# Performance work log

Hardware: AMD Instinct MI355X
Metric: run time of the kernel (lower is better)

## Reference

```python
import jax, jax.numpy as jnp
import numpy as np

WIN = 1022       # window_length == frame_length == fft_length
HOP = 256        # hop_length
SIG_LEN = 33216  # signal_length
FACTOR = 2       # downsampling factor
T_IN = 127       # input STFT frames
B = 64
L_OLA = (T_IN - 1) * HOP + WIN  # 33278, length produced by inverse_stft

# indices kept after the strided deletion (evens < SIG_LEN, plus OLA tail beyond SIG_LEN)
KEEP = np.concatenate([np.arange(0, SIG_LEN, FACTOR), np.arange(SIG_LEN, L_OLA)])
L_OUT = KEEP.shape[0]                # 16670
T_OUT = 1 + (L_OUT - WIN) // HOP     # 62 output STFT frames

def _hann(n):
    # periodic Hann, matches tf.signal.hann_window default
    return (0.5 - 0.5 * np.cos(2.0 * np.pi * np.arange(n) / n)).astype(np.float32)

def _synth_window():
    # tf.signal.inverse_stft_window_fn(HOP): w / overlap-added w^2 (periodic form)
    w = _hann(WIN)
    d = w * w
    overlaps = -(-WIN // HOP)
    d = np.pad(d, (0, overlaps * HOP - WIN))
    d = d.reshape(-1, HOP).sum(0)      # per-phase sum of squares
    d = np.tile(d, overlaps)[:WIN]
    return (w / d).astype(np.float32)

WINDOW = jnp.asarray(_hann(WIN))
SYNTH = jnp.asarray(_synth_window())
OLA_IDX = jnp.asarray((np.arange(T_IN)[:, None] * HOP + np.arange(WIN)[None, :]).reshape(-1))
FRAME_IDX = jnp.asarray(np.arange(T_OUT)[:, None] * HOP + np.arange(WIN)[None, :])
KEEP_J = jnp.asarray(KEEP)

def setup_inputs() -> dict:
    key = jax.random.key(0)
    return {"inputs": jax.random.normal(key, (B, 512, T_IN, 2), dtype=jnp.float32)}

def reference(inputs):
    # inputs: [B, 512, T, 2] (real/imag stacked STFT)
    stfts = jax.lax.complex(inputs[..., 0], inputs[..., 1])   # [B, 512, T]
    stfts = jnp.transpose(stfts, (0, 2, 1))                   # [B, T, 512]
    # inverse_stft: irfft per frame, apply synthesis window, overlap-add
    frames = jnp.fft.irfft(stfts, n=WIN, axis=-1) * SYNTH
    b = frames.shape[0]
    sig = jnp.zeros((b, L_OLA), frames.dtype).at[:, OLA_IDX].add(frames.reshape(b, -1))
    # strided index deletion (the unstack/del/stack loop) == single gather
    sig = sig[:, KEEP_J]                                      # [B, 16670]
    # forward STFT
    fr = sig[:, FRAME_IDX] * WINDOW
    S = jnp.fft.rfft(fr, n=WIN, axis=-1)                      # [B, T_OUT, 512]
    S = jnp.transpose(S, (0, 2, 1))                           # [B, 512, T_OUT]
    return jnp.stack([jnp.real(S), jnp.imag(S)], axis=-1)     # [B, 512, T_OUT, 2]
```

## Files before the change

### kernel.cpp

```cpp
#include <hip/hip_runtime.h>


#define WIN       1022
#define HOP       256
#define T_IN      127
#define NB        64
#define NPAD      1024
#define NE        512
#define T_OUT     62
#define HALF_KEPT 16608
#define L_USE     16638
#define ROWS1     8128
#define ROWS1P    8192
#define ROWS2     3968
#define ROWS2P    4096
#define TWO_PI_F  6.28318530717958647692f

typedef _Float16 half8 __attribute__((ext_vector_type(8)));
typedef float    f32x4 __attribute__((ext_vector_type(4)));

__global__ __launch_bounds__(256) void prep(const float* __restrict__ in,
                                            _Float16* __restrict__ M1T,
                                            _Float16* __restrict__ M2T,
                                            _Float16* __restrict__ A1) {
    __shared__ float lds[32 * 254];
    int bx = blockIdx.x, tid = threadIdx.x;
    const float cc = TWO_PI_F / (float)WIN;

    if (bx < 4096) {
        int idx = bx * 256 + tid, j = idx >> 10, kk = idx & 1023;
        if ((j & 1) && j < 961) return;
        float v = 0.f;
        if (j < WIN) {
            float w = 0.5f - 0.5f * __cosf(cc * (float)j);
            float dd = 0.f;
            int p = j & (HOP - 1);
            for (int r = 0; r < 4; ++r) {
                int ix = p + HOP * r;
                if (ix < WIN) {
                    float wi = 0.5f - 0.5f * __cosf(cc * (float)ix);
                    dd += wi * wi;
                }
            }
            float synth = w / dd;
            int k = kk >> 1, c = kk & 1;
            if (!(c == 1 && (k == 0 || k == 511))) {
                float a = (k == 0 || k == 511) ? (1.f / (float)WIN) : (2.f / (float)WIN);
                int m = (k * j) % WIN;
                float s, co;
                __sincosf((float)m * cc, &s, &co);
                v = a * synth * (c == 0 ? co : -s);
            }
        }
        M1T[idx] = (_Float16)v;
        return;
    }
    if (bx < 8192) {
        int idx = (bx - 4096) * 256 + tid, col = idx >> 10, j = idx & 1023;
        float v = 0.f;
        if (j < WIN) {
            float w = 0.5f - 0.5f * __cosf(cc * (float)j);
            int k = col >> 1, c = col & 1;
            int m = (k * j) % WIN;
            float s, co;
            __sincosf((float)m * cc, &s, &co);
            v = w * (c == 0 ? co : -s);
        }
        M2T[idx] = (_Float16)v;
        return;
    }
    int bx2 = bx - 8192;
    int kt = bx2 >> 6, b = bx2 & 63;
    const float* base = in + ((size_t)b * 512 + kt * 32) * (T_IN * 2);
    for (int idx2 = tid; idx2 < 32 * 254; idx2 += 256)
        lds[idx2] = base[idx2];
    __syncthreads();
    for (int f = tid; f < T_IN * 64; f += 256) {
        int t = f >> 6, l = f & 63;
        int dk = l >> 1, c = l & 1;
        A1[(size_t)(b * T_IN + t) * NPAD + kt * 64 + l] =
            (_Float16)lds[dk * 254 + t * 2 + c];
    }
}


__device__ __forceinline__ void stage16(const void* g, void* l) {
    __builtin_amdgcn_global_load_lds(
        (const __attribute__((address_space(1))) unsigned int*)g,
        (__attribute__((address_space(3))) unsigned int*)l, 16, 0, 0);
}

template <bool G2, int BPITCH, int CPITCH>
__global__ __launch_bounds__(256) void gemm_mfma(const _Float16* __restrict__ A,
                                                 const _Float16* __restrict__ B0,
                                                 void* __restrict__ Cv) {
    __shared__ __align__(16) _Float16 As[128 * 32];
    __shared__ __align__(16) _Float16 Bs[64 * 32];

    int tid  = threadIdx.x;
    int lane = tid & 63, wave = tid >> 6;
    int quad = lane >> 4, l16 = lane & 15;
    int rowOff = (wave >> 1) * 64, colOff = (wave & 1) * 32;
    int rowBase = blockIdx.y * 128, colBase = blockIdx.x * 64;

    int r = tid >> 2, ko = (tid & 3) * 8;
    const _Float16* Arow0 = A + (size_t)(rowBase + r) * NPAD + ko;
    const _Float16* Arow1 = Arow0 + (size_t)64 * NPAD;
    const _Float16* Brow  = B0 + (size_t)(colBase + r) * BPITCH + ko;

    f32x4 acc[4][2] = {};

    for (int k0 = 0; k0 < NPAD; k0 += 32) {
        stage16(Arow0 + k0, As + r * 32 + ko);
        stage16(Arow1 + k0, As + (64 + r) * 32 + ko);
        stage16(Brow  + k0, Bs + r * 32 + ko);
        __syncthreads();

        half8 af[4], bf[2];
#pragma unroll
        for (int i = 0; i < 4; ++i)
            af[i] = *(const half8*)&As[(rowOff + i * 16 + l16) * 32 + quad * 8];
#pragma unroll
        for (int j = 0; j < 2; ++j)
            bf[j] = *(const half8*)&Bs[(colOff + j * 16 + l16) * 32 + quad * 8];
#pragma unroll
        for (int i = 0; i < 4; ++i)
#pragma unroll
            for (int j = 0; j < 2; ++j)
                acc[i][j] = __builtin_amdgcn_mfma_f32_16x16x32_f16(af[i], bf[j], acc[i][j], 0, 0, 0);
        __syncthreads();
    }

#pragma unroll
    for (int i = 0; i < 4; ++i) {
#pragma unroll
        for (int j = 0; j < 2; ++j) {
            int col = colBase + colOff + j * 16 + l16;
#pragma unroll
            for (int rr = 0; rr < 4; ++rr) {
                int row = rowBase + rowOff + i * 16 + quad * 4 + rr;
                if (!G2) {
                    ((_Float16*)Cv)[(size_t)row * CPITCH + col] = (_Float16)acc[i][j][rr];
                } else if (row < ROWS2) {
                    int b = row / T_OUT, t2 = row % T_OUT;
                    int k = col >> 1, c = col & 1;
                    ((float*)Cv)[(((size_t)b * 512 + k) * T_OUT + t2) * 2 + c] = acc[i][j][rr];
                }
            }
        }
    }
}

__global__ void ola_pack(const _Float16* __restrict__ fe,
                         const _Float16* __restrict__ A1,
                         const _Float16* __restrict__ M1T,
                         _Float16* __restrict__ fr) {
    int i = blockIdx.x * 256 + threadIdx.x;
    int b = blockIdx.y;
    if (i >= L_USE) return;

    float v = 0.f;
    if (i < HALF_KEPT) {
        int tmin = (i > 510) ? ((i - 383) >> 7) : 0;
        int tmax = i >> 7; if (tmax > T_IN - 1) tmax = T_IN - 1;
        for (int t = tmin; t <= tmax; ++t)
            v += (float)fe[(size_t)(b * T_IN + t) * NE + (i - t * 128)];
    } else {
        int s = i + HALF_KEPT;
        int p = s - 32256;
        if (!(s & 1)) {
            v = (float)fe[(size_t)(b * T_IN + 126) * NE + (p >> 1)];
        } else {
            const _Float16* ar = A1 + (size_t)(b * T_IN + 126) * NPAD;
            const _Float16* mr = M1T + (size_t)p * NPAD;
            float a0 = 0.f;
            for (int k = 0; k < NPAD; k += 8) {
                half8 av = *(const half8*)&ar[k];
                half8 mv = *(const half8*)&mr[k];
#pragma unroll
                for (int u = 0; u < 8; ++u)
                    a0 += (float)av[u] * (float)mv[u];
            }
            v = a0;
        }
    }

    _Float16 hv = (_Float16)v;
    int t2min = (i > WIN - 1) ? ((i - (WIN - 1) + HOP - 1) >> 8) : 0;
    int t2max = i >> 8; if (t2max > T_OUT - 1) t2max = T_OUT - 1;
    for (int t2 = t2min; t2 <= t2max; ++t2)
        fr[(size_t)(b * T_OUT + t2) * NPAD + (i - t2 * HOP)] = hv;
}


extern "C" void kernel_launch(void* const* d_in, const int* in_sizes, int n_in,
                              void* d_out, int out_size, void* d_ws, size_t ws_size,
                              hipStream_t stream) {
    const float* in = (const float*)d_in[0];
    float* out = (float*)d_out;
    char* ws = (char*)d_ws;

    _Float16* M1T = (_Float16*)ws;
    _Float16* M2T = M1T + (size_t)NPAD * NPAD;
    _Float16* A1  = M2T + (size_t)NPAD * NPAD;
    _Float16* fr  = A1 + (size_t)ROWS1P * NPAD;
    _Float16* fe  = fr + (size_t)ROWS2P * NPAD;

    prep<<<9216, 256, 0, stream>>>(in, M1T, M2T, A1);
    gemm_mfma<false, 2 * NPAD, NE><<<dim3(NE / 64, ROWS1P / 128), 256, 0, stream>>>(A1, M1T, fe);
    ola_pack<<<dim3(65, NB), 256, 0, stream>>>(fe, A1, M1T, fr);
    gemm_mfma<true, NPAD, 0><<<dim3(NPAD / 64, ROWS2P / 128), 256, 0, stream>>>(fr, M2T, out);
}
```

Before: 156.5 us.

## Split GEMM K dimension across two blocks and widen K tile to 64

Both GEMMs are split-K over two halves using blockIdx.z. The first GEMM writes two partial fe buffers that ola_pack sums, and the second accumulates into the output with atomicAdd after a memset. The LDS K-tile doubles to 64, halving barrier count per K step. This doubles grid size to improve occupancy on the CU-rich GPU, at the cost of extra fe traffic, atomics, and a memset.

After: 281.8 us. +80.1%, slower.

```diff
diff --git a/kernel.cpp b/kernel.cpp
--- a/kernel.cpp
+++ b/kernel.cpp
@@ -90,44 +90,62 @@
         (__attribute__((address_space(3))) unsigned int*)l, 16, 0, 0);
 }
 
-template <bool G2, int BPITCH, int CPITCH>
+template <bool G2>
 __global__ __launch_bounds__(256) void gemm_mfma(const _Float16* __restrict__ A,
                                                  const _Float16* __restrict__ B0,
                                                  void* __restrict__ Cv) {
-    __shared__ __align__(16) _Float16 As[128 * 32];
-    __shared__ __align__(16) _Float16 Bs[64 * 32];
+    constexpr int BPITCH = G2 ? NPAD : 2 * NPAD;
+    __shared__ __align__(16) _Float16 As[128 * 64];
+    __shared__ __align__(16) _Float16 Bs[64 * 64];
 
     int tid  = threadIdx.x;
     int lane = tid & 63, wave = tid >> 6;
     int quad = lane >> 4, l16 = lane & 15;
     int rowOff = (wave >> 1) * 64, colOff = (wave & 1) * 32;
     int rowBase = blockIdx.y * 128, colBase = blockIdx.x * 64;
-
-    int r = tid >> 2, ko = (tid & 3) * 8;
-    const _Float16* Arow0 = A + (size_t)(rowBase + r) * NPAD + ko;
-    const _Float16* Arow1 = Arow0 + (size_t)64 * NPAD;
-    const _Float16* Brow  = B0 + (size_t)(colBase + r) * BPITCH + ko;
+    int kbase = blockIdx.z * NE;
+
+    const _Float16* Ag[4]; _Float16* Al[4];
+    const _Float16* Bg[2]; _Float16* Bl[2];
+#pragma unroll
+    for (int u = 0; u < 4; ++u) {
+        int f = u * 256 + tid, r = f >> 3, ko = (f & 7) * 8;
+        Ag[u] = A + (size_t)(rowBase + r) * NPAD + kbase + ko;
+        Al[u] = As + f * 8;
+    }
+#pragma unroll
+    for (int u = 0; u < 2; ++u) {
+        int f = u * 256 + tid, r = f >> 3, ko = (f & 7) * 8;
+        Bg[u] = B0 + (size_t)(colBase + r) * BPITCH + kbase + ko;
+        Bl[u] = Bs + f * 8;
+    }
 
     f32x4 acc[4][2] = {};
 
-    for (int k0 = 0; k0 < NPAD; k0 += 32) {
-        stage16(Arow0 + k0, As + r * 32 + ko);
-        stage16(Arow1 + k0, As + (64 + r) * 32 + ko);
-        stage16(Brow  + k0, Bs + r * 32 + ko);
+    for (int k0 = 0; k0 < NE; k0 += 64) {
+#pragma unroll
+        for (int u = 0; u < 4; ++u) stage16(Ag[u] + k0, Al[u]);
+#pragma unroll
+        for (int u = 0; u < 2; ++u) stage16(Bg[u] + k0, Bl[u]);
         __syncthreads();
 
-        half8 af[4], bf[2];
-#pragma unroll
-        for (int i = 0; i < 4; ++i)
-            af[i] = *(const half8*)&As[(rowOff + i * 16 + l16) * 32 + quad * 8];
-#pragma unroll
-        for (int j = 0; j < 2; ++j)
-            bf[j] = *(const half8*)&Bs[(colOff + j * 16 + l16) * 32 + quad * 8];
-#pragma unroll
-        for (int i = 0; i < 4; ++i)
+        half8 af[2][4], bf[2][2];
+#pragma unroll
+        for (int s = 0; s < 2; ++s) {
+#pragma unroll
+            for (int i = 0; i < 4; ++i)
+                af[s][i] = *(const half8*)&As[(rowOff + i * 16 + l16) * 64 + s * 32 + quad * 8];
 #pragma unroll
             for (int j = 0; j < 2; ++j)
-                acc[i][j] = __builtin_amdgcn_mfma_f32_16x16x32_f16(af[i], bf[j], acc[i][j], 0, 0, 0);
+                bf[s][j] = *(const half8*)&Bs[(colOff + j * 16 + l16) * 64 + s * 32 + quad * 8];
+        }
+#pragma unroll
+        for (int s = 0; s < 2; ++s)
+#pragma unroll
+            for (int i = 0; i < 4; ++i)
+#pragma unroll
+                for (int j = 0; j < 2; ++j)
+                    acc[i][j] = __builtin_amdgcn_mfma_f32_16x16x32_f16(af[s][i], bf[s][j], acc[i][j], 0, 0, 0);
         __syncthreads();
     }
 
@@ -140,18 +158,21 @@
             for (int rr = 0; rr < 4; ++rr) {
                 int row = rowBase + rowOff + i * 16 + quad * 4 + rr;
                 if (!G2) {
-                    ((_Float16*)Cv)[(size_t)row * CPITCH + col] = (_Float16)acc[i][j][rr];
+                    _Float16* fe = (_Float16*)Cv + (size_t)blockIdx.z * ROWS1P * NE;
+                    fe[(size_t)row * NE + col] = (_Float16)acc[i][j][rr];
                 } else if (row < ROWS2) {
                     int b = row / T_OUT, t2 = row % T_OUT;
                     int k = col >> 1, c = col & 1;
-                    ((float*)Cv)[(((size_t)b * 512 + k) * T_OUT + t2) * 2 + c] = acc[i][j][rr];
+                    atomicAdd((float*)Cv + (((size_t)b * 512 + k) * T_OUT + t2) * 2 + c,
+                              acc[i][j][rr]);
                 }
             }
         }
     }
 }
 
-__global__ void ola_pack(const _Float16* __restrict__ fe,
+__global__ void ola_pack(const _Float16* __restrict__ fe0,
+                         const _Float16* __restrict__ fe1,
                          const _Float16* __restrict__ A1,
                          const _Float16* __restrict__ M1T,
                          _Float16* __restrict__ fr) {
@@ -163,13 +184,16 @@
     if (i < HALF_KEPT) {
         int tmin = (i > 510) ? ((i - 383) >> 7) : 0;
         int tmax = i >> 7; if (tmax > T_IN - 1) tmax = T_IN - 1;
-        for (int t = tmin; t <= tmax; ++t)
-            v += (float)fe[(size_t)(b * T_IN + t) * NE + (i - t * 128)];
+        for (int t = tmin; t <= tmax; ++t) {
+            size_t idx = (size_t)(b * T_IN + t) * NE + (i - t * 128);
+            v += (float)fe0[idx] + (float)fe1[idx];
+        }
     } else {
         int s = i + HALF_KEPT;
         int p = s - 32256;
         if (!(s & 1)) {
-            v = (float)fe[(size_t)(b * T_IN + 126) * NE + (p >> 1)];
+            size_t idx = (size_t)(b * T_IN + 126) * NE + (p >> 1);
+            v = (float)fe0[idx] + (float)fe1[idx];
         } else {
             const _Float16* ar = A1 + (size_t)(b * T_IN + 126) * NPAD;
             const _Float16* mr = M1T + (size_t)p * NPAD;
@@ -206,8 +230,9 @@
     _Float16* fr  = A1 + (size_t)ROWS1P * NPAD;
     _Float16* fe  = fr + (size_t)ROWS2P * NPAD;
 
+    hipMemsetAsync(out, 0, (size_t)out_size * sizeof(float), stream);
     prep<<<9216, 256, 0, stream>>>(in, M1T, M2T, A1);
-    gemm_mfma<false, 2 * NPAD, NE><<<dim3(NE / 64, ROWS1P / 128), 256, 0, stream>>>(A1, M1T, fe);
-    ola_pack<<<dim3(65, NB), 256, 0, stream>>>(fe, A1, M1T, fr);
-    gemm_mfma<true, NPAD, 0><<<dim3(NPAD / 64, ROWS2P / 128), 256, 0, stream>>>(fr, M2T, out);
-}
+    gemm_mfma<false><<<dim3(NE / 64, ROWS1P / 128, 2), 256, 0, stream>>>(A1, M1T, fe);
+    ola_pack<<<dim3(65, NB), 256, 0, stream>>>(fe, fe + (size_t)ROWS1P * NE, A1, M1T, fr);
+    gemm_mfma<true><<<dim3(NPAD / 64, ROWS2P / 128, 2), 256, 0, stream>>>(fr, M2T, out);
+}
```
